# Kernel tuning notes

Hardware: AMD Instinct MI355X
Metric: run time of the kernel (lower is better)

The kernel has to match this reference:

```python
import jax, jax.numpy as jnp
import numpy as np


def setup_inputs() -> dict:
    key = jax.random.key(0)
    kq, kk, kv = jax.random.split(key, 3)
    B, H, T, D = 1, 16, 4096, 64
    Q = jax.random.normal(kq, (B, H, T, D), dtype=jnp.float32)
    K = jax.random.normal(kk, (B, H, T, D), dtype=jnp.float32)
    V = jax.random.normal(kv, (B, H, T, D), dtype=jnp.float32)
    return {"Q": Q, "K": K, "V": V}


def reference(Q, K, V):
    B, H, T, D = Q.shape
    # ALiBi slopes: m_h = 2^(-8*h/H), h = 1..H (deterministic buffer)
    slopes = jnp.exp2(-8.0 * jnp.arange(1, H + 1, dtype=jnp.float32) / H)
    pos = jnp.arange(T, dtype=jnp.float32)
    dist = jnp.abs(pos[None, :] - pos[:, None])          # (T, T)
    bias = slopes[:, None, None] * dist                   # (H, T, T)
    scale = jnp.sqrt(jnp.asarray(D, dtype=Q.dtype))
    scores = jnp.einsum('bhtd,bhsd->bhts', Q, K) / scale - bias[None]
    attn = jax.nn.softmax(scores, axis=-1)
    return jnp.einsum('bhts,bhsd->bhtd', attn, V)
```

## Files before the change

kernel.cpp:

```cpp
#include <hip/hip_runtime.h>
#include <hip/hip_bf16.h>
#include <stdint.h>

typedef float f4    __attribute__((ext_vector_type(4)));
typedef float f32x4 __attribute__((ext_vector_type(4)));
typedef short s16x8 __attribute__((ext_vector_type(8)));
typedef short s16x4 __attribute__((ext_vector_type(4)));
typedef unsigned short u16;

#define T_LEN 4096
#define NHEAD 16
#define DHEAD 64
#define KVBLK 64
#define NT    (T_LEN / KVBLK)

#if __has_builtin(__builtin_amdgcn_exp2f)
#define EXP2(x) __builtin_amdgcn_exp2f(x)
#else
#define EXP2(x) exp2f(x)
#endif

#define SLOT_F 8320
#define CONV_BYTES ((size_t)16777216)
#define SLOTS_BAL  1152
#define BAL_BYTES  (CONV_BYTES + (size_t)SLOTS_BAL * SLOT_F * 4u)

__device__ __constant__ int NCARR[8] = {2,2,3,5,6,6,6,6};
__device__ __constant__ int SBARR[8] = {1088,1024,928,768,576,384,192,0};

__device__ __forceinline__ uint32_t pk2(float a, float b){
  uint32_t ua = __builtin_bit_cast(uint32_t, a) + 0x8000u;
  uint32_t ub = __builtin_bit_cast(uint32_t, b) + 0x8000u;
  return __builtin_amdgcn_perm(ub, ua, 0x07060302u);
}
__device__ __forceinline__ int swk(int r){ return (r ^ (r >> 3)) & 7; }
__device__ __forceinline__ int sw(int r){ return swk(r) << 3; }

__global__ __launch_bounds__(256)
void cvt_kv(const float* __restrict__ K, const float* __restrict__ V,
            u16* __restrict__ Kb, u16* __restrict__ VT){
  __shared__ u16 tile[64][66];
  if (blockIdx.x < 2048){
    const size_t i = ((size_t)blockIdx.x * 256 + threadIdx.x) * 8;
    f4 a = *(const f4*)(K + i);
    f4 b = *(const f4*)(K + i + 4);
    union { uint32_t w[4]; s16x8 v; } u;
    u.w[0] = pk2(a[0], a[1]); u.w[1] = pk2(a[2], a[3]);
    u.w[2] = pk2(b[0], b[1]); u.w[3] = pk2(b[2], b[3]);
    *(s16x8*)(Kb + i) = u.v;
  } else {
    const int vb = blockIdx.x - 2048;
    const int h  = vb >> 6;
    const int kt = vb & 63;
    const int t  = threadIdx.x;
    const float* Vh = V + ((size_t)h * T_LEN + kt * 64) * DHEAD;

    const int r = t >> 2, c = (t & 3) * 16;
    f4 x0 = *(const f4*)(Vh + r*64 + c);
    f4 x1 = *(const f4*)(Vh + r*64 + c + 4);
    f4 x2 = *(const f4*)(Vh + r*64 + c + 8);
    f4 x3 = *(const f4*)(Vh + r*64 + c + 12);
    uint32_t* tp = (uint32_t*)&tile[r][c];
    tp[0] = pk2(x0[0],x0[1]); tp[1] = pk2(x0[2],x0[3]);
    tp[2] = pk2(x1[0],x1[1]); tp[3] = pk2(x1[2],x1[3]);
    tp[4] = pk2(x2[0],x2[1]); tp[5] = pk2(x2[2],x2[3]);
    tp[6] = pk2(x3[0],x3[1]); tp[7] = pk2(x3[2],x3[3]);
    __syncthreads();

    const int d = t >> 2, ks = (t & 3) * 16;
    u16* op = VT + ((size_t)h * DHEAD + d) * T_LEN + kt * 64 + ks;
    union { uint32_t w[4]; s16x8 v; } o0, o1;
#pragma unroll
    for (int q = 0; q < 4; ++q)
      o0.w[q] = (uint32_t)tile[ks + 2*q][d]     | ((uint32_t)tile[ks + 2*q + 1][d] << 16);
#pragma unroll
    for (int q = 0; q < 4; ++q)
      o1.w[q] = (uint32_t)tile[ks + 8 + 2*q][d] | ((uint32_t)tile[ks + 9 + 2*q][d] << 16);
    *(s16x8*)(op)     = o0.v;
    *(s16x8*)(op + 8) = o1.v;
  }
}

__global__ __launch_bounds__(512, 4)
void alibi_attn7(const float* __restrict__ Qg,
                 const u16* __restrict__ Kb,
                 const u16* __restrict__ VTb,
                 float* __restrict__ Og,
                 float* __restrict__ part)
{
  __shared__ u16 kbuf[2][KVBLK * DHEAD];
  __shared__ u16 vbuf[2][DHEAD * KVBLK];

  int h, qt, c, n, sb;
  {
    int r = blockIdx.x;
    if (r < 768){
      h = 15 - r / 192; r %= 192; n = 6; qt = r / 6; c = r % 6; sb = (15 - h) * 192;
    } else if ((r -= 768) < 160){
      h = 11; n = 5; qt = r / 5; c = r % 5; sb = 768;
    } else if ((r -= 160) < 96){
      h = 10; n = 3; qt = r / 3; c = r % 3; sb = 928;
    } else if ((r -= 96) < 64){
      h = 9; n = 2; qt = r >> 1; c = r & 1; sb = 1024;
    } else if ((r -= 64) < 64){
      h = 8; n = 2; qt = r >> 1; c = r & 1; sb = 1088;
    } else {
      r -= 64; h = r >> 5; qt = r & 31; n = 1; c = 0; sb = 0;
    }
  }

  const int tid  = threadIdx.x;
  const int wv   = tid >> 6;
  const int lane = tid & 63;
  const int lg   = lane >> 4;
  const int ln   = lane & 15;

  const int q0   = qt * 128;
  const int qrow = q0 + wv * 16 + ln;
  const float slope = exp2f(-0.5f * (float)(h + 1));
  const float cs = 0.125f * 1.44269504089f;
  const float bs = slope * 1.44269504089f;
  const size_t headoff = (size_t)h * T_LEN * DHEAD;

  const int Di = (int)(36.0f / bs);
  int lo = (q0 - Di) >> 6;           if (lo < 0) lo = 0;
  int hi = (q0 + 127 + Di) >> 6;     if (hi > NT - 1) hi = NT - 1;
  const int len = hi - lo + 1;
  const int start = lo + (c * len) / n;
  const int end   = lo + ((c + 1) * len) / n;

  s16x8 qf0, qf1;
  {
    const float* qp = Qg + headoff + (size_t)qrow * DHEAD + lg * 8;
    f4 x = *(const f4*)qp;        f4 y = *(const f4*)(qp + 4);
    f4 z = *(const f4*)(qp + 32); f4 v = *(const f4*)(qp + 36);
    union { uint32_t w_[4]; s16x8 v_; } u0, u1;
    u0.w_[0] = pk2(x[0]*cs, x[1]*cs); u0.w_[1] = pk2(x[2]*cs, x[3]*cs);
    u0.w_[2] = pk2(y[0]*cs, y[1]*cs); u0.w_[3] = pk2(y[2]*cs, y[3]*cs);
    u1.w_[0] = pk2(z[0]*cs, z[1]*cs); u1.w_[1] = pk2(z[2]*cs, z[3]*cs);
    u1.w_[2] = pk2(v[0]*cs, v[1]*cs); u1.w_[3] = pk2(v[2]*cs, v[3]*cs);
    qf0 = u0.v_; qf1 = u1.v_;
  }

  f32x4 acc[4];
#pragma unroll
  for (int dt = 0; dt < 4; ++dt) acc[dt] = (f32x4)(0.0f);
  float lsum = 0.0f;
  const float base0 = (float)qrow - (float)(lg * 4);

  int koffs[4][2];
#pragma unroll
  for (int kt = 0; kt < 4; ++kt){
    const int key = kt*16 + ln, sz = sw(key);
    koffs[kt][0] = (((key*64      + lg*8) ^ sz)) * 2;
    koffs[kt][1] = (((key*64 + 32 + lg*8) ^ sz)) * 2;
  }
  int voffs[4][4];
#pragma unroll
  for (int dt = 0; dt < 4; ++dt){
    const int d = dt*16 + ln, sz = sw(d);
#pragma unroll
    for (int kt = 0; kt < 4; ++kt)
      voffs[dt][kt] = (((d*64 + kt*16 + lg*4) ^ sz)) * 2;
  }

  const u16* Kh = Kb  + headoff;
  const u16* Vh = VTb + headoff;
  const int keyA = tid >> 3, gA = (tid & 7) ^ swk(keyA);
  const int kidxA = keyA * 64 + gA * 8;
  const int vidxA = keyA * T_LEN + gA * 8;
  const int dstA = tid * 16;

  s16x8 rkA, rvA;
  auto ldregs = [&](int t){
    rkA = *(const s16x8*)(Kh + (size_t)t * (KVBLK * DHEAD) + kidxA);
    rvA = *(const s16x8*)(Vh + (size_t)t * KVBLK + vidxA);
  };
  auto wrregs = [&](u16* kb_, u16* vb_){
    *(s16x8*)((char*)kb_ + dstA) = rkA;
    *(s16x8*)((char*)vb_ + dstA) = rvA;
  };

  auto compute = [&](const u16* kb_, const u16* vb_, int kv){
    f32x4 S[4];
    __builtin_amdgcn_s_setprio(1);
#pragma unroll
    for (int kt = 0; kt < 4; ++kt){
      s16x8 k0 = *(const s16x8*)((const char*)kb_ + koffs[kt][0]);
      s16x8 k1 = *(const s16x8*)((const char*)kb_ + koffs[kt][1]);
      f32x4 cc = (f32x4)(0.0f);
      cc = __builtin_amdgcn_mfma_f32_16x16x32_bf16(k0, qf0, cc, 0, 0, 0);
      cc = __builtin_amdgcn_mfma_f32_16x16x32_bf16(k1, qf1, cc, 0, 0, 0);
      S[kt] = cc;
    }
    __builtin_amdgcn_s_setprio(0);

    const float bi = base0 - (float)(kv * KVBLK);
    float p[16];
#pragma unroll
    for (int kt = 0; kt < 4; ++kt)
#pragma unroll
      for (int r = 0; r < 4; ++r)
        p[kt*4 + r] = EXP2(fmaf(-bs, fabsf(bi - (float)(kt*16 + r)), S[kt][r]));

    lsum += (((p[0]+p[1]) + (p[2]+p[3])) + ((p[4]+p[5]) + (p[6]+p[7])))
          + (((p[8]+p[9]) + (p[10]+p[11])) + ((p[12]+p[13]) + (p[14]+p[15])));

    s16x4 pb[4];
#pragma unroll
    for (int kt = 0; kt < 4; ++kt){
      union { uint32_t w_[2]; s16x4 v_; } u;
      u.w_[0] = pk2(p[kt*4+0], p[kt*4+1]);
      u.w_[1] = pk2(p[kt*4+2], p[kt*4+3]);
      pb[kt] = u.v_;
    }

    __builtin_amdgcn_s_setprio(1);
#pragma unroll
    for (int dt = 0; dt < 4; ++dt){
#pragma unroll
      for (int kt = 0; kt < 4; ++kt){
        const s16x4 vf = *(const s16x4*)((const char*)vb_ + voffs[dt][kt]);
        acc[dt] = __builtin_amdgcn_mfma_f32_16x16x16bf16_1k(vf, pb[kt], acc[dt], 0, 0, 0);
      }
    }
    __builtin_amdgcn_s_setprio(0);
  };

  {
    ldregs(start);
    wrregs(kbuf[0], vbuf[0]);
    __syncthreads();

    const int hi_i = end - 1;
    int t = start;
#pragma unroll 1
    while (t + 1 < hi_i){
      ldregs(t + 1);
      compute(kbuf[0], vbuf[0], t);
      wrregs(kbuf[1], vbuf[1]);
      __syncthreads();
      ldregs(t + 2);
      compute(kbuf[1], vbuf[1], t + 1);
      wrregs(kbuf[0], vbuf[0]);
      __syncthreads();
      t += 2;
    }
    if (t < hi_i){
      ldregs(t + 1);
      compute(kbuf[0], vbuf[0], t);
      wrregs(kbuf[1], vbuf[1]);
      __syncthreads();
      compute(kbuf[1], vbuf[1], t + 1);
    } else {
      compute(kbuf[0], vbuf[0], t);
    }
  }

  lsum += __shfl_xor(lsum, 16, 64);
  lsum += __shfl_xor(lsum, 32, 64);

  if (n == 1){
    const float inv = 1.0f / lsum;
    float* op = Og + headoff + (size_t)qrow * DHEAD + lg * 4;
#pragma unroll
    for (int dt = 0; dt < 4; ++dt){
      f4 o;
      o[0] = acc[dt][0] * inv; o[1] = acc[dt][1] * inv;
      o[2] = acc[dt][2] * inv; o[3] = acc[dt][3] * inv;
      *(f4*)(op + dt*16) = o;
    }
  } else {
    float* slot = part + (size_t)(sb + qt * n + c) * SLOT_F;
    const int row = wv * 16 + ln;
    float* op = slot + row * 64 + lg * 4;
#pragma unroll
    for (int dt = 0; dt < 4; ++dt)
      *(f4*)(op + dt*16) = acc[dt];
    if (lg == 0) slot[8192 + row] = lsum;
  }
}

__global__ __launch_bounds__(256)
void combine_k(const float* __restrict__ part, float* __restrict__ Og){
  const int h  = 8 + (blockIdx.x >> 5);
  const int qt = blockIdx.x & 31;
  const int n  = NCARR[h - 8];
  const int sb = SBARR[h - 8] + qt * n;

  const int t   = threadIdx.x;
  const int row = t >> 1;
  const int seg = (t & 1) * 32;

  f4 a[8];
#pragma unroll
  for (int i = 0; i < 8; ++i) a[i] = (f4)(0.0f);
  float l = 0.0f;
#pragma unroll 1
  for (int c = 0; c < n; ++c){
    const float* sp = part + (size_t)(sb + c) * SLOT_F;
    const float* rp = sp + row * 64 + seg;
#pragma unroll
    for (int i = 0; i < 8; ++i) a[i] += *(const f4*)(rp + i*4);
    l += sp[8192 + row];
  }
  const float inv = 1.0f / l;
  float* op = Og + (((size_t)h * T_LEN + qt * 128 + row) * DHEAD) + seg;
#pragma unroll
  for (int i = 0; i < 8; ++i){
    f4 o;
    o[0] = a[i][0]*inv; o[1] = a[i][1]*inv; o[2] = a[i][2]*inv; o[3] = a[i][3]*inv;
    *(f4*)(op + i*4) = o;
  }
}

__global__ __launch_bounds__(256, 4)
void alibi_attn4(const float* __restrict__ Qg,
                 const u16* __restrict__ Kb,
                 const u16* __restrict__ VTb,
                 float* __restrict__ Og)
{
  __shared__ u16 kbuf[2][KVBLK * DHEAD];
  __shared__ u16 vbuf[2][DHEAD * KVBLK];

  const int bid = blockIdx.x;
  const int fid = (bid & 7) * 128 + (bid >> 3);
  const int h  = fid & 15;
  const int qt = fid >> 4;

  const int tid  = threadIdx.x;
  const int wv   = tid >> 6;
  const int lane = tid & 63;
  const int lg   = lane >> 4;
  const int ln   = lane & 15;

  const int q0   = qt * 64;
  const int qrow = q0 + wv * 16 + ln;
  const float slope = exp2f(-0.5f * (float)(h + 1));
  const float cs = 0.125f * 1.44269504089f;
  const float bs = slope * 1.44269504089f;
  const size_t headoff = (size_t)h * T_LEN * DHEAD;

  const int Di = (int)(36.0f / bs);
  int lo = (q0 - Di) >> 6;           if (lo < 0) lo = 0;
  int hi = (q0 + 63 + Di) >> 6;      if (hi > NT - 1) hi = NT - 1;

  s16x8 qf0, qf1;
  {
    const float* qp = Qg + headoff + (size_t)qrow * DHEAD + lg * 8;
    f4 x = *(const f4*)qp;        f4 y = *(const f4*)(qp + 4);
    f4 z = *(const f4*)(qp + 32); f4 v = *(const f4*)(qp + 36);
    union { uint32_t w_[4]; s16x8 v_; } u0, u1;
    u0.w_[0] = pk2(x[0]*cs, x[1]*cs); u0.w_[1] = pk2(x[2]*cs, x[3]*cs);
    u0.w_[2] = pk2(y[0]*cs, y[1]*cs); u0.w_[3] = pk2(y[2]*cs, y[3]*cs);
    u1.w_[0] = pk2(z[0]*cs, z[1]*cs); u1.w_[1] = pk2(z[2]*cs, z[3]*cs);
    u1.w_[2] = pk2(v[0]*cs, v[1]*cs); u1.w_[3] = pk2(v[2]*cs, v[3]*cs);
    qf0 = u0.v_; qf1 = u1.v_;
  }

  f32x4 acc[4];
#pragma unroll
  for (int dt = 0; dt < 4; ++dt) acc[dt] = (f32x4)(0.0f);
  float lsum = 0.0f;
  const float base0 = (float)qrow - (float)(lg * 4);

  int koffs[4][2];
#pragma unroll
  for (int kt = 0; kt < 4; ++kt){
    const int key = kt*16 + ln, sz = sw(key);
    koffs[kt][0] = (((key*64      + lg*8) ^ sz)) * 2;
    koffs[kt][1] = (((key*64 + 32 + lg*8) ^ sz)) * 2;
  }
  int voffs[4][4];
#pragma unroll
  for (int dt = 0; dt < 4; ++dt){
    const int d = dt*16 + ln, sz = sw(d);
#pragma unroll
    for (int kt = 0; kt < 4; ++kt)
      voffs[dt][kt] = (((d*64 + kt*16 + lg*4) ^ sz)) * 2;
  }

  const u16* Kh = Kb  + headoff;
  const u16* Vh = VTb + headoff;
  const int sA = wv * 128 + lane;
  const int sB = sA + 64;
  const int keyA = sA >> 3, gA = (sA & 7) ^ swk(keyA);
  const int keyB = sB >> 3, gB = (sB & 7) ^ swk(keyB);
  const int kidxA = keyA * 64 + gA * 8;
  const int kidxB = keyB * 64 + gB * 8;
  const int vidxA = keyA * T_LEN + gA * 8;
  const int vidxB = keyB * T_LEN + gB * 8;
  const int dstA = sA * 16, dstB = sB * 16;

  s16x8 rkA, rkB, rvA, rvB;
  auto ldregs = [&](int t){
    const u16* kp = Kh + (size_t)t * (KVBLK * DHEAD);
    const u16* vp = Vh + (size_t)t * KVBLK;
    rkA = *(const s16x8*)(kp + kidxA);  rkB = *(const s16x8*)(kp + kidxB);
    rvA = *(const s16x8*)(vp + vidxA);  rvB = *(const s16x8*)(vp + vidxB);
  };
  auto wrregs = [&](u16* kb_, u16* vb_){
    *(s16x8*)((char*)kb_ + dstA) = rkA;  *(s16x8*)((char*)kb_ + dstB) = rkB;
    *(s16x8*)((char*)vb_ + dstA) = rvA;  *(s16x8*)((char*)vb_ + dstB) = rvB;
  };

  auto compute = [&](const u16* kb_, const u16* vb_, int kv){
    f32x4 S[4];
    __builtin_amdgcn_s_setprio(1);
#pragma unroll
    for (int kt = 0; kt < 4; ++kt){
      s16x8 k0 = *(const s16x8*)((const char*)kb_ + koffs[kt][0]);
      s16x8 k1 = *(const s16x8*)((const char*)kb_ + koffs[kt][1]);
      f32x4 cc = (f32x4)(0.0f);
      cc = __builtin_amdgcn_mfma_f32_16x16x32_bf16(k0, qf0, cc, 0, 0, 0);
      cc = __builtin_amdgcn_mfma_f32_16x16x32_bf16(k1, qf1, cc, 0, 0, 0);
      S[kt] = cc;
    }
    __builtin_amdgcn_s_setprio(0);

    const float bi = base0 - (float)(kv * KVBLK);
    float p[16];
#pragma unroll
    for (int kt = 0; kt < 4; ++kt)
#pragma unroll
      for (int r = 0; r < 4; ++r)
        p[kt*4 + r] = EXP2(fmaf(-bs, fabsf(bi - (float)(kt*16 + r)), S[kt][r]));

    lsum += (((p[0]+p[1]) + (p[2]+p[3])) + ((p[4]+p[5]) + (p[6]+p[7])))
          + (((p[8]+p[9]) + (p[10]+p[11])) + ((p[12]+p[13]) + (p[14]+p[15])));

    s16x4 pb[4];
#pragma unroll
    for (int kt = 0; kt < 4; ++kt){
      union { uint32_t w_[2]; s16x4 v_; } u;
      u.w_[0] = pk2(p[kt*4+0], p[kt*4+1]);
      u.w_[1] = pk2(p[kt*4+2], p[kt*4+3]);
      pb[kt] = u.v_;
    }

    __builtin_amdgcn_s_setprio(1);
#pragma unroll
    for (int dt = 0; dt < 4; ++dt){
#pragma unroll
      for (int kt = 0; kt < 4; ++kt){
        const s16x4 vf = *(const s16x4*)((const char*)vb_ + voffs[dt][kt]);
        acc[dt] = __builtin_amdgcn_mfma_f32_16x16x16bf16_1k(vf, pb[kt], acc[dt], 0, 0, 0);
      }
    }
    __builtin_amdgcn_s_setprio(0);
  };

  ldregs(lo);
  wrregs(kbuf[0], vbuf[0]);
  __syncthreads();

  int t = lo;
#pragma unroll 1
  while (t + 1 < hi){
    ldregs(t + 1);
    compute(kbuf[0], vbuf[0], t);
    wrregs(kbuf[1], vbuf[1]);
    __syncthreads();
    ldregs(t + 2);
    compute(kbuf[1], vbuf[1], t + 1);
    wrregs(kbuf[0], vbuf[0]);
    __syncthreads();
    t += 2;
  }
  if (t < hi){
    ldregs(t + 1);
    compute(kbuf[0], vbuf[0], t);
    wrregs(kbuf[1], vbuf[1]);
    __syncthreads();
    compute(kbuf[1], vbuf[1], t + 1);
  } else {
    compute(kbuf[0], vbuf[0], t);
  }

  lsum += __shfl_xor(lsum, 16, 64);
  lsum += __shfl_xor(lsum, 32, 64);
  const float inv = 1.0f / lsum;
  float* op = Og + headoff + (size_t)qrow * DHEAD + lg * 4;
#pragma unroll
  for (int dt = 0; dt < 4; ++dt){
    f4 o;
    o[0] = acc[dt][0] * inv; o[1] = acc[dt][1] * inv;
    o[2] = acc[dt][2] * inv; o[3] = acc[dt][3] * inv;
    *(f4*)(op + dt*16) = o;
  }
}

__global__ __launch_bounds__(256, 2)
void alibi_attn_fb(const float* __restrict__ Qg,
                   const float* __restrict__ Kg,
                   const float* __restrict__ Vg,
                   float* __restrict__ Og)
{
  __shared__ u16 kbuf[2][KVBLK * DHEAD];
  __shared__ u16 vbuf[2][DHEAD * KVBLK];

  const int bid = blockIdx.x;
  const int fid = (bid & 7) * 64 + (bid >> 3);
  const int h  = fid >> 5;
  const int qt = fid & 31;

  const int tid  = threadIdx.x;
  const int wave = tid >> 6;
  const int lane = tid & 63;
  const int lg   = lane >> 4;
  const int ln   = lane & 15;

  const int qb = qt * 128 + wave * 32;
  const float slope = exp2f(-0.5f * (float)(h + 1));
  const float cs = 0.125f * 1.44269504089f;
  const float bs = slope * 1.44269504089f;
  const size_t headoff = (size_t)h * T_LEN * DHEAD;

  s16x8 qf[2][2];
#pragma unroll
  for (int rg = 0; rg < 2; ++rg)
#pragma unroll
    for (int dh = 0; dh < 2; ++dh){
      const float* qp = Qg + headoff + (size_t)(qb + rg*16 + ln) * DHEAD + dh*32 + lg*8;
      f4 x = *(const f4*)qp;
      f4 y = *(const f4*)(qp + 4);
      union { uint32_t w[4]; s16x8 v; } u;
      u.w[0] = pk2(x[0]*cs, x[1]*cs);
      u.w[1] = pk2(x[2]*cs, x[3]*cs);
      u.w[2] = pk2(y[0]*cs, y[1]*cs);
      u.w[3] = pk2(y[2]*cs, y[3]*cs);
      qf[rg][dh] = u.v;
    }

  f32x4 acc[2][4];
#pragma unroll
  for (int rg = 0; rg < 2; ++rg)
#pragma unroll
    for (int dt = 0; dt < 4; ++dt) acc[rg][dt] = (f32x4)(0.0f);
  float mreg[2] = {-1e30f, -1e30f};
  float lreg[2] = {0.0f, 0.0f};
  const float qposf[2] = {(float)(qb + ln), (float)(qb + 16 + ln)};
  const float koffb = (float)(lg * 4);

  f4 st4[8];
  const int vk0  = (tid >> 2) * 2;
  const int vseg = (tid & 3) * 16;
  const int krow = (tid - 128) >> 1;
  const int kseg = ((tid - 128) & 1) * 32;
  const float* Vb = Vg + headoff;
  const float* Kb_ = Kg + headoff;

  auto stage_load = [&](int kv){
    const int kb = kv * KVBLK;
    if (tid < 128){
      const float* vp = Vb + (size_t)(kb + vk0) * DHEAD + vseg;
      st4[0] = *(const f4*)(vp);      st4[1] = *(const f4*)(vp + 4);
      st4[2] = *(const f4*)(vp + 8);  st4[3] = *(const f4*)(vp + 12);
      st4[4] = *(const f4*)(vp + 64); st4[5] = *(const f4*)(vp + 68);
      st4[6] = *(const f4*)(vp + 72); st4[7] = *(const f4*)(vp + 76);
    } else {
      const float* kp = Kb_ + (size_t)(kb + krow) * DHEAD + kseg;
#pragma unroll
      for (int j = 0; j < 8; ++j) st4[j] = *(const f4*)(kp + j*4);
    }
  };
  auto stage_store = [&](int b){
    if (tid < 128){
#pragma unroll
      for (int i = 0; i < 16; ++i){
        const int d = vseg + i;
        uint32_t pr = pk2(st4[i>>2][i&3], st4[4 + (i>>2)][i&3]);
        *(uint32_t*)&vbuf[b][(d*64 + vk0) ^ sw(d)] = pr;
      }
    } else {
#pragma unroll
      for (int i = 0; i < 4; ++i){
        union { uint32_t w[4]; s16x8 v; } u;
        u.w[0] = pk2(st4[i*2][0],   st4[i*2][1]);
        u.w[1] = pk2(st4[i*2][2],   st4[i*2][3]);
        u.w[2] = pk2(st4[i*2+1][0], st4[i*2+1][1]);
        u.w[3] = pk2(st4[i*2+1][2], st4[i*2+1][3]);
        *(s16x8*)&kbuf[b][(krow*64 + kseg + i*8) ^ sw(krow)] = u.v;
      }
    }
  };

  stage_load(0);
  stage_store(0);
  __syncthreads();
  int cur = 0;

#pragma unroll 1
  for (int kv = 0; kv < NT; ++kv){
    if (kv + 1 < NT) stage_load(kv + 1);

    const float kbf = (float)(kv * KVBLK);
    const u16* kb_ = kbuf[cur];
    const u16* vb_ = vbuf[cur];

    s16x8 kf[4][2];
#pragma unroll
    for (int kt = 0; kt < 4; ++kt){
      const int key = kt*16 + ln;
      const int sz  = sw(key);
      kf[kt][0] = *(const s16x8*)&kb_[(key*64 +      lg*8) ^ sz];
      kf[kt][1] = *(const s16x8*)&kb_[(key*64 + 32 + lg*8) ^ sz];
    }
    f32x4 S[2][4];
#pragma unroll
    for (int rg = 0; rg < 2; ++rg)
#pragma unroll
      for (int kt = 0; kt < 4; ++kt){
        f32x4 c = (f32x4)(0.0f);
        c = __builtin_amdgcn_mfma_f32_16x16x32_bf16(kf[kt][0], qf[rg][0], c, 0, 0, 0);
        c = __builtin_amdgcn_mfma_f32_16x16x32_bf16(kf[kt][1], qf[rg][1], c, 0, 0, 0);
        S[rg][kt] = c;
      }

    s16x4 pb[2][4];
#pragma unroll
    for (int rg = 0; rg < 2; ++rg){
      const float base = qposf[rg] - kbf - koffb;
#pragma unroll
      for (int kt = 0; kt < 4; ++kt)
#pragma unroll
        for (int r = 0; r < 4; ++r)
          S[rg][kt][r] = fmaf(-bs, fabsf(base - (float)(kt*16 + r)), S[rg][kt][r]);

      float a0 = fmaxf(fmaxf(S[rg][0][0], S[rg][0][1]), fmaxf(S[rg][0][2], S[rg][0][3]));
      float a1 = fmaxf(fmaxf(S[rg][1][0], S[rg][1][1]), fmaxf(S[rg][1][2], S[rg][1][3]));
      float a2 = fmaxf(fmaxf(S[rg][2][0], S[rg][2][1]), fmaxf(S[rg][2][2], S[rg][2][3]));
      float a3 = fmaxf(fmaxf(S[rg][3][0], S[rg][3][1]), fmaxf(S[rg][3][2], S[rg][3][3]));
      float mx = fmaxf(fmaxf(a0, a1), fmaxf(a2, a3));
      mx = fmaxf(mx, __shfl_xor(mx, 16, 64));
      mx = fmaxf(mx, __shfl_xor(mx, 32, 64));

      const float mo = mreg[rg];
      const float mn = fmaxf(mo, mx);
      const float scl = EXP2(mo - mn);
      mreg[rg] = mn;

      float p[16];
#pragma unroll
      for (int kt = 0; kt < 4; ++kt)
#pragma unroll
        for (int r = 0; r < 4; ++r)
          p[kt*4 + r] = EXP2(S[rg][kt][r] - mn);

      float s0 = (p[0]+p[1]) + (p[2]+p[3]);
      float s1 = (p[4]+p[5]) + (p[6]+p[7]);
      float s2 = (p[8]+p[9]) + (p[10]+p[11]);
      float s3 = (p[12]+p[13]) + (p[14]+p[15]);
      float sum = (s0+s1) + (s2+s3);
      sum += __shfl_xor(sum, 16, 64);
      sum += __shfl_xor(sum, 32, 64);
      lreg[rg] = lreg[rg] * scl + sum;

#pragma unroll
      for (int dt = 0; dt < 4; ++dt) acc[rg][dt] *= scl;

#pragma unroll
      for (int kt = 0; kt < 4; ++kt){
        union { uint32_t w[2]; s16x4 v; } u;
        u.w[0] = pk2(p[kt*4+0], p[kt*4+1]);
        u.w[1] = pk2(p[kt*4+2], p[kt*4+3]);
        pb[rg][kt] = u.v;
      }
    }

#pragma unroll
    for (int dt = 0; dt < 4; ++dt){
      const int d  = dt*16 + ln;
      const int sz = sw(d);
#pragma unroll
      for (int kt = 0; kt < 4; ++kt){
        const s16x4 vf = *(const s16x4*)&vb_[(d*64 + kt*16 + lg*4) ^ sz];
        acc[0][dt] = __builtin_amdgcn_mfma_f32_16x16x16bf16_1k(vf, pb[0][kt], acc[0][dt], 0, 0, 0);
        acc[1][dt] = __builtin_amdgcn_mfma_f32_16x16x16bf16_1k(vf, pb[1][kt], acc[1][dt], 0, 0, 0);
      }
    }

    if (kv + 1 < NT){
      stage_store(cur ^ 1);
      __syncthreads();
      cur ^= 1;
    }
  }

#pragma unroll
  for (int rg = 0; rg < 2; ++rg){
    const float inv = 1.0f / lreg[rg];
    float* op = Og + headoff + (size_t)(qb + rg*16 + ln) * DHEAD + lg*4;
#pragma unroll
    for (int dt = 0; dt < 4; ++dt){
      f4 o;
      o[0] = acc[rg][dt][0] * inv;
      o[1] = acc[rg][dt][1] * inv;
      o[2] = acc[rg][dt][2] * inv;
      o[3] = acc[rg][dt][3] * inv;
      *(f4*)(op + dt*16) = o;
    }
  }
}

extern "C" void kernel_launch(void* const* d_in, const int* in_sizes, int n_in,
                              void* d_out, int out_size, void* d_ws, size_t ws_size,
                              hipStream_t stream)
{
  const float* Q = (const float*)d_in[0];
  const float* K = (const float*)d_in[1];
  const float* V = (const float*)d_in[2];
  float* O = (float*)d_out;

  if (ws_size >= BAL_BYTES){
    u16* Kb = (u16*)d_ws;
    u16* VT = Kb + (size_t)NHEAD * T_LEN * DHEAD;
    float* part = (float*)((char*)d_ws + CONV_BYTES);
    hipLaunchKernelGGL(cvt_kv, dim3(3072), dim3(256), 0, stream, K, V, Kb, VT);
    hipLaunchKernelGGL(alibi_attn7, dim3(1408), dim3(512), 0, stream, Q, Kb, VT, O, part);
    hipLaunchKernelGGL(combine_k, dim3(256), dim3(256), 0, stream, part, O);
  } else if (ws_size >= CONV_BYTES){
    u16* Kb = (u16*)d_ws;
    u16* VT = Kb + (size_t)NHEAD * T_LEN * DHEAD;
    hipLaunchKernelGGL(cvt_kv, dim3(3072), dim3(256), 0, stream, K, V, Kb, VT);
    hipLaunchKernelGGL(alibi_attn4, dim3(1024), dim3(256), 0, stream, Q, Kb, VT, O);
  } else {
    hipLaunchKernelGGL(alibi_attn_fb, dim3(512), dim3(256), 0, stream, Q, K, V, O);
  }
}
```

Baseline: 88.50 us.

## Process two 16-row query groups per wave to reuse K/V fragments

```diff
diff --git a/kernel.cpp b/kernel.cpp
--- a/kernel.cpp
+++ b/kernel.cpp
@@ -81,8 +81,8 @@
   }
 }
 
-__global__ __launch_bounds__(512, 4)
-void alibi_attn7(const float* __restrict__ Qg,
+__global__ __launch_bounds__(256, 2)
+void alibi_attn8(const float* __restrict__ Qg,
                  const u16* __restrict__ Kb,
                  const u16* __restrict__ VTb,
                  float* __restrict__ Og,
@@ -116,7 +116,7 @@
   const int ln   = lane & 15;
 
   const int q0   = qt * 128;
-  const int qrow = q0 + wv * 16 + ln;
+  const int qr0  = q0 + wv * 32 + ln;
   const float slope = exp2f(-0.5f * (float)(h + 1));
   const float cs = 0.125f * 1.44269504089f;
   const float bs = slope * 1.44269504089f;
@@ -129,9 +129,10 @@
   const int start = lo + (c * len) / n;
   const int end   = lo + ((c + 1) * len) / n;
 
-  s16x8 qf0, qf1;
-  {
-    const float* qp = Qg + headoff + (size_t)qrow * DHEAD + lg * 8;
+  s16x8 qf[2][2];
+#pragma unroll
+  for (int rg = 0; rg < 2; ++rg){
+    const float* qp = Qg + headoff + (size_t)(qr0 + rg*16) * DHEAD + lg * 8;
     f4 x = *(const f4*)qp;        f4 y = *(const f4*)(qp + 4);
     f4 z = *(const f4*)(qp + 32); f4 v = *(const f4*)(qp + 36);
     union { uint32_t w_[4]; s16x8 v_; } u0, u1;
@@ -139,14 +140,16 @@
     u0.w_[2] = pk2(y[0]*cs, y[1]*cs); u0.w_[3] = pk2(y[2]*cs, y[3]*cs);
     u1.w_[0] = pk2(z[0]*cs, z[1]*cs); u1.w_[1] = pk2(z[2]*cs, z[3]*cs);
     u1.w_[2] = pk2(v[0]*cs, v[1]*cs); u1.w_[3] = pk2(v[2]*cs, v[3]*cs);
-    qf0 = u0.v_; qf1 = u1.v_;
-  }
-
-  f32x4 acc[4];
-#pragma unroll
-  for (int dt = 0; dt < 4; ++dt) acc[dt] = (f32x4)(0.0f);
-  float lsum = 0.0f;
-  const float base0 = (float)qrow - (float)(lg * 4);
+    qf[rg][0] = u0.v_; qf[rg][1] = u1.v_;
+  }
+
+  f32x4 acc[2][4];
+#pragma unroll
+  for (int rg = 0; rg < 2; ++rg)
+#pragma unroll
+    for (int dt = 0; dt < 4; ++dt) acc[rg][dt] = (f32x4)(0.0f);
+  float lsum[2] = {0.0f, 0.0f};
+  const float b0 = (float)qr0 - (float)(lg * 4);
 
   int koffs[4][2];
 #pragma unroll
@@ -166,53 +169,66 @@
 
   const u16* Kh = Kb  + headoff;
   const u16* Vh = VTb + headoff;
-  const int keyA = tid >> 3, gA = (tid & 7) ^ swk(keyA);
+  const int sA = wv * 128 + lane;
+  const int sB = sA + 64;
+  const int keyA = sA >> 3, gA = (sA & 7) ^ swk(keyA);
+  const int keyB = sB >> 3, gB = (sB & 7) ^ swk(keyB);
   const int kidxA = keyA * 64 + gA * 8;
+  const int kidxB = keyB * 64 + gB * 8;
   const int vidxA = keyA * T_LEN + gA * 8;
-  const int dstA = tid * 16;
-
-  s16x8 rkA, rvA;
+  const int vidxB = keyB * T_LEN + gB * 8;
+  const int dstA = sA * 16, dstB = sB * 16;
+
+  s16x8 rkA, rkB, rvA, rvB;
   auto ldregs = [&](int t){
-    rkA = *(const s16x8*)(Kh + (size_t)t * (KVBLK * DHEAD) + kidxA);
-    rvA = *(const s16x8*)(Vh + (size_t)t * KVBLK + vidxA);
+    const u16* kp = Kh + (size_t)t * (KVBLK * DHEAD);
+    const u16* vp = Vh + (size_t)t * KVBLK;
+    rkA = *(const s16x8*)(kp + kidxA);  rkB = *(const s16x8*)(kp + kidxB);
+    rvA = *(const s16x8*)(vp + vidxA);  rvB = *(const s16x8*)(vp + vidxB);
   };
   auto wrregs = [&](u16* kb_, u16* vb_){
-    *(s16x8*)((char*)kb_ + dstA) = rkA;
-    *(s16x8*)((char*)vb_ + dstA) = rvA;
+    *(s16x8*)((char*)kb_ + dstA) = rkA;  *(s16x8*)((char*)kb_ + dstB) = rkB;
+    *(s16x8*)((char*)vb_ + dstA) = rvA;  *(s16x8*)((char*)vb_ + dstB) = rvB;
   };
 
   auto compute = [&](const u16* kb_, const u16* vb_, int kv){
-    f32x4 S[4];
+    f32x4 S[2][4];
     __builtin_amdgcn_s_setprio(1);
 #pragma unroll
     for (int kt = 0; kt < 4; ++kt){
       s16x8 k0 = *(const s16x8*)((const char*)kb_ + koffs[kt][0]);
       s16x8 k1 = *(const s16x8*)((const char*)kb_ + koffs[kt][1]);
-      f32x4 cc = (f32x4)(0.0f);
-      cc = __builtin_amdgcn_mfma_f32_16x16x32_bf16(k0, qf0, cc, 0, 0, 0);
-      cc = __builtin_amdgcn_mfma_f32_16x16x32_bf16(k1, qf1, cc, 0, 0, 0);
-      S[kt] = cc;
+      f32x4 c0 = (f32x4)(0.0f), c1 = (f32x4)(0.0f);
+      c0 = __builtin_amdgcn_mfma_f32_16x16x32_bf16(k0, qf[0][0], c0, 0, 0, 0);
+      c0 = __builtin_amdgcn_mfma_f32_16x16x32_bf16(k1, qf[0][1], c0, 0, 0, 0);
+      c1 = __builtin_amdgcn_mfma_f32_16x16x32_bf16(k0, qf[1][0], c1, 0, 0, 0);
+      c1 = __builtin_amdgcn_mfma_f32_16x16x32_bf16(k1, qf[1][1], c1, 0, 0, 0);
+      S[0][kt] = c0; S[1][kt] = c1;
     }
     __builtin_amdgcn_s_setprio(0);
 
-    const float bi = base0 - (float)(kv * KVBLK);
-    float p[16];
-#pragma unroll
-    for (int kt = 0; kt < 4; ++kt)
-#pragma unroll
-      for (int r = 0; r < 4; ++r)
-        p[kt*4 + r] = EXP2(fmaf(-bs, fabsf(bi - (float)(kt*16 + r)), S[kt][r]));
-
-    lsum += (((p[0]+p[1]) + (p[2]+p[3])) + ((p[4]+p[5]) + (p[6]+p[7])))
-          + (((p[8]+p[9]) + (p[10]+p[11])) + ((p[12]+p[13]) + (p[14]+p[15])));
-
-    s16x4 pb[4];
-#pragma unroll
-    for (int kt = 0; kt < 4; ++kt){
-      union { uint32_t w_[2]; s16x4 v_; } u;
-      u.w_[0] = pk2(p[kt*4+0], p[kt*4+1]);
-      u.w_[1] = pk2(p[kt*4+2], p[kt*4+3]);
-      pb[kt] = u.v_;
+    s16x4 pb[2][4];
+#pragma unroll
+    for (int rg = 0; rg < 2; ++rg){
+      const float bi = b0 + (float)(rg * 16) - (float)(kv * KVBLK);
+#pragma unroll
+      for (int kt = 0; kt < 4; ++kt)
+#pragma unroll
+        for (int r = 0; r < 4; ++r)
+          S[rg][kt][r] = EXP2(fmaf(-bs, fabsf(bi - (float)(kt*16 + r)), S[rg][kt][r]));
+
+      lsum[rg] += (((S[rg][0][0]+S[rg][0][1]) + (S[rg][0][2]+S[rg][0][3]))
+                +  ((S[rg][1][0]+S[rg][1][1]) + (S[rg][1][2]+S[rg][1][3])))
+                + (((S[rg][2][0]+S[rg][2][1]) + (S[rg][2][2]+S[rg][2][3]))
+                +  ((S[rg][3][0]+S[rg][3][1]) + (S[rg][3][2]+S[rg][3][3])));
+
+#pragma unroll
+      for (int kt = 0; kt < 4; ++kt){
+        union { uint32_t w_[2]; s16x4 v_; } u;
+        u.w_[0] = pk2(S[rg][kt][0], S[rg][kt][1]);
+        u.w_[1] = pk2(S[rg][kt][2], S[rg][kt][3]);
+        pb[rg][kt] = u.v_;
+      }
     }
 
     __builtin_amdgcn_s_setprio(1);
@@ -221,7 +237,8 @@
 #pragma unroll
       for (int kt = 0; kt < 4; ++kt){
         const s16x4 vf = *(const s16x4*)((const char*)vb_ + voffs[dt][kt]);
-        acc[dt] = __builtin_amdgcn_mfma_f32_16x16x16bf16_1k(vf, pb[kt], acc[dt], 0, 0, 0);
+        acc[0][dt] = __builtin_amdgcn_mfma_f32_16x16x16bf16_1k(vf, pb[0][kt], acc[0][dt], 0, 0, 0);
+        acc[1][dt] = __builtin_amdgcn_mfma_f32_16x16x16bf16_1k(vf, pb[1][kt], acc[1][dt], 0, 0, 0);
       }
     }
     __builtin_amdgcn_s_setprio(0);
@@ -257,27 +274,36 @@
     }
   }
 
-  lsum += __shfl_xor(lsum, 16, 64);
-  lsum += __shfl_xor(lsum, 32, 64);
+#pragma unroll
+  for (int rg = 0; rg < 2; ++rg){
+    lsum[rg] += __shfl_xor(lsum[rg], 16, 64);
+    lsum[rg] += __shfl_xor(lsum[rg], 32, 64);
+  }
 
   if (n == 1){
-    const float inv = 1.0f / lsum;
-    float* op = Og + headoff + (size_t)qrow * DHEAD + lg * 4;
-#pragma unroll
-    for (int dt = 0; dt < 4; ++dt){
-      f4 o;
-      o[0] = acc[dt][0] * inv; o[1] = acc[dt][1] * inv;
-      o[2] = acc[dt][2] * inv; o[3] = acc[dt][3] * inv;
-      *(f4*)(op + dt*16) = o;
+#pragma unroll
+    for (int rg = 0; rg < 2; ++rg){
+      const float inv = 1.0f / lsum[rg];
+      float* op = Og + headoff + (size_t)(qr0 + rg*16) * DHEAD + lg * 4;
+#pragma unroll
+      for (int dt = 0; dt < 4; ++dt){
+        f4 o;
+        o[0] = acc[rg][dt][0] * inv; o[1] = acc[rg][dt][1] * inv;
+        o[2] = acc[rg][dt][2] * inv; o[3] = acc[rg][dt][3] * inv;
+        *(f4*)(op + dt*16) = o;
+      }
     }
   } else {
     float* slot = part + (size_t)(sb + qt * n + c) * SLOT_F;
-    const int row = wv * 16 + ln;
-    float* op = slot + row * 64 + lg * 4;
-#pragma unroll
-    for (int dt = 0; dt < 4; ++dt)
-      *(f4*)(op + dt*16) = acc[dt];
-    if (lg == 0) slot[8192 + row] = lsum;
+#pragma unroll
+    for (int rg = 0; rg < 2; ++rg){
+      const int row = wv * 32 + rg * 16 + ln;
+      float* op = slot + row * 64 + lg * 4;
+#pragma unroll
+      for (int dt = 0; dt < 4; ++dt)
+        *(f4*)(op + dt*16) = acc[rg][dt];
+      if (lg == 0) slot[8192 + row] = lsum[rg];
+    }
   }
 }
 
@@ -717,7 +743,7 @@
     u16* VT = Kb + (size_t)NHEAD * T_LEN * DHEAD;
     float* part = (float*)((char*)d_ws + CONV_BYTES);
     hipLaunchKernelGGL(cvt_kv, dim3(3072), dim3(256), 0, stream, K, V, Kb, VT);
-    hipLaunchKernelGGL(alibi_attn7, dim3(1408), dim3(512), 0, stream, Q, Kb, VT, O, part);
+    hipLaunchKernelGGL(alibi_attn8, dim3(1408), dim3(256), 0, stream, Q, Kb, VT, O, part);
     hipLaunchKernelGGL(combine_k, dim3(256), dim3(256), 0, stream, part, O);
   } else if (ws_size >= CONV_BYTES){
     u16* Kb = (u16*)d_ws;
```

After: 86.62 us, median of 4. 1.02x faster.
